# Kernel tuning notes

Hardware: AMD Instinct MI355X
Metric: run time of the kernel (lower is better)

## Reference

```python
import jax, jax.numpy as jnp
import numpy as np

EMBED_DIM = 1024
NUM_HEADS = 16
HEAD_DIM = EMBED_DIM // NUM_HEADS
BATCH = 2
SEQ = 2048


def setup_inputs() -> dict:
    key = jax.random.key(0)
    ks = jax.random.split(key, 10)
    s = 1.0 / np.sqrt(EMBED_DIM)
    inp = {
        "query": jax.random.normal(ks[0], (BATCH, SEQ, EMBED_DIM), jnp.float32),
        # Linear weights stored as [in, out] (y = x @ W + b)
        "wq": jax.random.normal(ks[1], (EMBED_DIM, EMBED_DIM), jnp.float32) * s,
        "bq": jnp.zeros((EMBED_DIM,), jnp.float32),
        "wk": jax.random.normal(ks[2], (EMBED_DIM, EMBED_DIM), jnp.float32) * s,
        "bk": jnp.zeros((EMBED_DIM,), jnp.float32),
        "wv": jax.random.normal(ks[3], (EMBED_DIM, EMBED_DIM), jnp.float32) * s,
        "bv": jnp.zeros((EMBED_DIM,), jnp.float32),
        "wo": jax.random.normal(ks[4], (EMBED_DIM, EMBED_DIM), jnp.float32) * s,
        "bo": jnp.zeros((EMBED_DIM,), jnp.float32),
        "temperature": jnp.float32(HEAD_DIM),  # learnable temperature, init = head_dim
    }
    return inp


def reference(query, wq, bq, wk, bk, wv, bv, wo, bo, temperature):
    B, S, E = query.shape
    # self-attention: key = value = query
    Q = (query @ wq + bq).reshape(B, S, NUM_HEADS, HEAD_DIM).transpose(0, 2, 1, 3)
    K = (query @ wk + bk).reshape(B, S, NUM_HEADS, HEAD_DIM).transpose(0, 2, 1, 3)
    V = (query @ wv + bv).reshape(B, S, NUM_HEADS, HEAD_DIM).transpose(0, 2, 1, 3)
    # squared Euclidean distances: ||q||^2 + ||k||^2 - 2<q,k>
    q_sq = jnp.sum(Q * Q, axis=-1, keepdims=True)          # (B,H,Sq,1)
    k_sq = jnp.sum(K * K, axis=-1, keepdims=True)          # (B,H,Sk,1)
    qk = jnp.einsum("bhqd,bhkd->bhqk", Q, K)
    d_sq = jnp.maximum(q_sq + jnp.swapaxes(k_sq, -2, -1) - 2.0 * qk, 0.0)
    attn = jax.nn.softmax(-d_sq / temperature, axis=-1)    # (B,H,Sq,Sk)
    out = jnp.einsum("bhqk,bhkd->bhqd", attn, V)
    out = out.transpose(0, 2, 1, 3).reshape(B, S, E)
    return out @ wo + bo
```

## Files before the change

kernel.cpp:

```cpp
#include <hip/hip_runtime.h>
#include <stdint.h>
#include <stddef.h>


#define LOG2E 1.44269504088896f

typedef __attribute__((ext_vector_type(8))) short bf16x8;
typedef __attribute__((ext_vector_type(4))) short bf16x4;
typedef __attribute__((ext_vector_type(4))) float f32x4;
typedef __attribute__((ext_vector_type(4))) unsigned short u16x4;

__device__ __forceinline__ unsigned short f2b(float f) {
  union { float f; unsigned int u; } x; x.f = f;
  unsigned int u = x.u;
  u += 0x7fffu + ((u >> 16) & 1u);
  return (unsigned short)(u >> 16);
}
__device__ __forceinline__ float b2f(unsigned short s) {
  union { unsigned int u; float f; } x; x.u = ((unsigned int)s) << 16;
  return x.f;
}
__device__ __forceinline__ unsigned int fbits(float f) {
  union { float f; unsigned int u; } x; x.f = f; return x.u;
}

#define GLD_LDS(g, l) __builtin_amdgcn_global_load_lds( \
    (const __attribute__((address_space(1))) void*)(g), \
    (__attribute__((address_space(3))) void*)(l), 16, 0, 0)

__global__ void prep_kernel(const float* __restrict__ X,
                            const float* __restrict__ wq, const float* __restrict__ wk,
                            const float* __restrict__ wv, const float* __restrict__ wo,
                            unsigned short* __restrict__ Xb,
                            unsigned short* __restrict__ WTqkv, unsigned short* __restrict__ WTo) {
  int z = blockIdx.z;
  if (z == 4) {
    size_t base = ((size_t)(blockIdx.y * 16 + blockIdx.x)) * 16384;
    #pragma unroll
    for (int j = 0; j < 16; ++j) {
      size_t i = base + (size_t)(j * 256 + threadIdx.x) * 4;
      f32x4 v = *(const f32x4*)&X[i];
      u16x4 o;
      #pragma unroll
      for (int k = 0; k < 4; ++k) o[k] = f2b(v[k]);
      *(u16x4*)&Xb[i] = o;
    }
    return;
  }
  __shared__ float tile[64][65];
  const float* src = (z == 0) ? wq : (z == 1) ? wk : (z == 2) ? wv : wo;
  unsigned short* dst = (z < 3) ? (WTqkv + (size_t)z * 1024 * 1024) : WTo;
  int k0 = blockIdx.y * 64, n0 = blockIdx.x * 64;
  int rr = threadIdx.x >> 6, cc = threadIdx.x & 63;
  #pragma unroll
  for (int p = 0; p < 16; ++p) {
    int row = p * 4 + rr;
    tile[row][cc] = src[(size_t)(k0 + row) * 1024 + n0 + cc];
  }
  __syncthreads();
  #pragma unroll
  for (int p = 0; p < 16; ++p) {
    int row = p * 4 + rr;
    dst[(size_t)(n0 + row) * 1024 + k0 + cc] = f2b(tile[cc][row]);
  }
}

__global__ __launch_bounds__(256, 3) void gemm_qkv_kernel(
    const unsigned short* __restrict__ X, const unsigned short* __restrict__ WT,
    const float* __restrict__ bq, const float* __restrict__ bk, const float* __restrict__ bv,
    unsigned short* __restrict__ Qb, unsigned short* __restrict__ Kb,
    unsigned short* __restrict__ VTo, float* __restrict__ qs2, float* __restrict__ ks2) {
  __shared__ unsigned short As[2 * 128 * 32];
  __shared__ unsigned short Bs[2 * 128 * 32];
  const int t = threadIdx.x, w = t >> 6, lane = t & 63;
  const int r = lane & 15, q4 = lane >> 4;
  const int m0 = blockIdx.y * 128, n0 = blockIdx.x * 128;
  const int wr = (w >> 1) * 64, wc = (w & 1) * 64;
  const unsigned short* Xg = X + (size_t)m0 * 1024;
  const unsigned short* Wg = WT + (size_t)n0 * 1024;
  f32x4 acc[4][4] = {};
  for (int k0 = 0; k0 < 1024; k0 += 64) {
    #pragma unroll
    for (int g = 0; g < 4; ++g) {
      int slot = g * 256 + t;
      int kh = slot >> 9, row = (slot >> 2) & 127, ko = (slot & 3) * 8;
      GLD_LDS(Xg + (size_t)row * 1024 + k0 + kh * 32 + ko, &As[(g * 256 + w * 64) * 8]);
      GLD_LDS(Wg + (size_t)row * 1024 + k0 + kh * 32 + ko, &Bs[(g * 256 + w * 64) * 8]);
    }
    __syncthreads();
    #pragma unroll
    for (int kh = 0; kh < 2; ++kh) {
      bf16x8 af[4], bfr[4];
      #pragma unroll
      for (int mf = 0; mf < 4; ++mf)
        af[mf] = *(const bf16x8*)&As[kh * 4096 + (wr + mf * 16 + r) * 32 + q4 * 8];
      #pragma unroll
      for (int nf = 0; nf < 4; ++nf)
        bfr[nf] = *(const bf16x8*)&Bs[kh * 4096 + (wc + nf * 16 + r) * 32 + q4 * 8];
      #pragma unroll
      for (int mf = 0; mf < 4; ++mf)
        #pragma unroll
        for (int nf = 0; nf < 4; ++nf)
          acc[mf][nf] = __builtin_amdgcn_mfma_f32_16x16x32_bf16(af[mf], bfr[nf], acc[mf][nf], 0, 0, 0);
    }
    __syncthreads();
  }
  const int nblk = n0 >> 10;
  if (nblk < 2) {
    const float* bias = (nblk == 0) ? bq : bk;
    unsigned short* OutB = (nblk == 0) ? Qb : Kb;
    float* S2 = (nblk == 0) ? qs2 : ks2;
    const int nc0 = n0 & 1023;
    float s2a[4][4] = {};
    #pragma unroll
    for (int nf = 0; nf < 4; ++nf) {
      int n = nc0 + wc + nf * 16 + r;
      float bb = bias[n];
      #pragma unroll
      for (int mf = 0; mf < 4; ++mf) {
        int m = m0 + wr + mf * 16 + q4 * 4;
        f32x4 v = acc[mf][nf];
        #pragma unroll
        for (int i = 0; i < 4; ++i) {
          unsigned short os = f2b(v[i] + bb);
          OutB[(size_t)(m + i) * 1024 + n] = os;
          float xb = b2f(os);
          s2a[mf][i] += xb * xb;
        }
      }
    }
    #pragma unroll
    for (int mf = 0; mf < 4; ++mf)
      #pragma unroll
      for (int i = 0; i < 4; ++i) {
        float v = s2a[mf][i];
        v += __shfl_xor(v, 1, 64);
        v += __shfl_xor(v, 2, 64);
        v += __shfl_xor(v, 4, 64);
        v += __shfl_xor(v, 8, 64);
        s2a[mf][i] = v;
      }
    if (r == 0) {
      int hh = (nc0 + wc) >> 6;
      #pragma unroll
      for (int mf = 0; mf < 4; ++mf) {
        int m = m0 + wr + mf * 16 + q4 * 4;
        int bb2 = m >> 11, ss = m & 2047;
        #pragma unroll
        for (int i = 0; i < 4; ++i)
          S2[(size_t)(bb2 * 16 + hh) * 2048 + ss + i] = s2a[mf][i];
      }
    }
  } else {
    const int c0 = n0 - 2048;
    #pragma unroll
    for (int nf = 0; nf < 4; ++nf) {
      int c = c0 + wc + nf * 16 + r;
      float bb = bv[c];
      int h = c >> 6, d = c & 63;
      #pragma unroll
      for (int mf = 0; mf < 4; ++mf) {
        int m = m0 + wr + mf * 16 + q4 * 4;
        int b = m >> 11, s = m & 2047;
        f32x4 v = acc[mf][nf];
        u16x4 pk;
        #pragma unroll
        for (int i = 0; i < 4; ++i) pk[i] = f2b(v[i] + bb);
        *(u16x4*)&VTo[((size_t)((b * 16 + h) * 64 + d)) * 2048 + s] = pk;
      }
    }
  }
}

__global__ __launch_bounds__(256, 2) void flash_kernel(
    const unsigned short* __restrict__ Qb, const unsigned short* __restrict__ Kb,
    const unsigned short* __restrict__ VT, const float* __restrict__ qs2,
    const float* __restrict__ ks2, const float* __restrict__ temp,
    unsigned short* __restrict__ AO) {
  __shared__ unsigned short Ks[2][64 * 64];
  __shared__ unsigned short Vs[2][64 * 64];
  const int t = threadIdx.x, w = t >> 6, lane = t & 63;
  const int r = lane & 15, q4 = lane >> 4;
  const int bh = blockIdx.y, b = bh >> 4, h = bh & 15;
  const int q0 = blockIdx.x * 128;
  const float scale = LOG2E / temp[0];
  const float cc = 2.0f * scale;

  bf16x8 qf[2][2];
  #pragma unroll
  for (int mf = 0; mf < 2; ++mf) {
    int sq = q0 + w * 32 + mf * 16 + r;
    const unsigned short* qp = Qb + (size_t)(b * 2048 + sq) * 1024 + h * 64;
    #pragma unroll
    for (int ks = 0; ks < 2; ++ks) qf[mf][ks] = *(const bf16x8*)(qp + ks * 32 + q4 * 8);
  }
  float qs_s[2];
  #pragma unroll
  for (int mf = 0; mf < 2; ++mf)
    qs_s[mf] = scale * qs2[bh * 2048 + q0 + w * 32 + mf * 16 + r];

  f32x4 accO[2][4] = {};
  f32x4 lsum[2] = {};
  bf16x8 ones;
  #pragma unroll
  for (int j = 0; j < 8; ++j) ones[j] = (short)0x3F80;

  const unsigned short* Kg = Kb + ((size_t)b * 2048) * 1024 + h * 64;
  const unsigned short* Vg = VT + ((size_t)bh * 64) * 2048;
  const float* kqb = ks2 + bh * 2048;

  #pragma unroll
  for (int g = 0; g < 2; ++g) {
    int slot = g * 256 + t;
    int khalf = slot >> 8, key = (slot >> 2) & 63, ko = (slot & 3) * 8;
    GLD_LDS(Kg + (size_t)key * 1024 + khalf * 32 + ko, &Ks[0][slot * 8]);
    int dd = slot >> 3, gg = (slot & 7) ^ (dd & 7);
    GLD_LDS(Vg + (size_t)dd * 2048 + gg * 8, &Vs[0][slot * 8]);
  }
  f32x4 kq[4];
  #pragma unroll
  for (int kfm = 0; kfm < 4; ++kfm) {
    f32x4 raw = *(const f32x4*)&kqb[kfm * 16 + q4 * 4];
    #pragma unroll
    for (int i = 0; i < 4; ++i) kq[kfm][i] = scale * raw[i];
  }

  #pragma unroll 2
  for (int c = 0; c < 32; ++c) {
    const int buf = c & 1;
    __syncthreads();
    f32x4 kqn[4];
    if (c < 31) {
      #pragma unroll
      for (int g = 0; g < 2; ++g) {
        int slot = g * 256 + t;
        int khalf = slot >> 8, key = (slot >> 2) & 63, ko = (slot & 3) * 8;
        GLD_LDS(Kg + (size_t)((c + 1) * 64 + key) * 1024 + khalf * 32 + ko,
                &Ks[buf ^ 1][slot * 8]);
        int dd = slot >> 3, gg = (slot & 7) ^ (dd & 7);
        GLD_LDS(Vg + (size_t)dd * 2048 + (c + 1) * 64 + gg * 8,
                &Vs[buf ^ 1][slot * 8]);
      }
      #pragma unroll
      for (int kfm = 0; kfm < 4; ++kfm) {
        f32x4 raw = *(const f32x4*)&kqb[(c + 1) * 64 + kfm * 16 + q4 * 4];
        #pragma unroll
        for (int i = 0; i < 4; ++i) kqn[kfm][i] = scale * raw[i];
      }
    }

    f32x4 accST[4][2] = {};
    #pragma unroll
    for (int ks = 0; ks < 2; ++ks) {
      #pragma unroll
      for (int kfm = 0; kfm < 4; ++kfm) {
        bf16x8 ka = *(const bf16x8*)&Ks[buf][(ks * 64 + kfm * 16 + r) * 32 + q4 * 8];
        accST[kfm][0] = __builtin_amdgcn_mfma_f32_16x16x32_bf16(ka, qf[0][ks], accST[kfm][0], 0, 0, 0);
        accST[kfm][1] = __builtin_amdgcn_mfma_f32_16x16x32_bf16(ka, qf[1][ks], accST[kfm][1], 0, 0, 0);
      }
    }

    bf16x8 pf[2][2];
    #pragma unroll
    for (int cb = 0; cb < 2; ++cb) {
      #pragma unroll
      for (int mf = 0; mf < 2; ++mf) {
        unsigned int dw[4];
        #pragma unroll
        for (int half = 0; half < 2; ++half) {
          int kfm = cb * 2 + half;
          float pp[4];
          #pragma unroll
          for (int i = 0; i < 4; ++i) {
            float u = __builtin_fmaf(cc, accST[kfm][mf][i], -(kq[kfm][i] + qs_s[mf]));
            pp[i] = __builtin_amdgcn_exp2f(fminf(u, 0.f));
          }
          dw[half * 2 + 0] = (fbits(pp[0]) >> 16) | (fbits(pp[1]) & 0xFFFF0000u);
          dw[half * 2 + 1] = (fbits(pp[2]) >> 16) | (fbits(pp[3]) & 0xFFFF0000u);
        }
        union { unsigned int d[4]; bf16x8 v; } cv;
        cv.d[0] = dw[0]; cv.d[1] = dw[1]; cv.d[2] = dw[2]; cv.d[3] = dw[3];
        pf[cb][mf] = cv.v;
      }
    }

    #pragma unroll
    for (int cb = 0; cb < 2; ++cb) {
      #pragma unroll
      for (int mf = 0; mf < 2; ++mf)
        lsum[mf] = __builtin_amdgcn_mfma_f32_16x16x32_bf16(pf[cb][mf], ones, lsum[mf], 0, 0, 0);
      #pragma unroll
      for (int df = 0; df < 4; ++df) {
        int dloc = df * 16 + r;
        int e0 = (cb * 4 + (q4 >> 1)) ^ (r & 7);
        int e1 = (cb * 4 + 2 + (q4 >> 1)) ^ (r & 7);
        bf16x4 v0 = *(const bf16x4*)&Vs[buf][dloc * 64 + e0 * 8 + (q4 & 1) * 4];
        bf16x4 v1 = *(const bf16x4*)&Vs[buf][dloc * 64 + e1 * 8 + (q4 & 1) * 4];
        bf16x8 vb = __builtin_shufflevector(v0, v1, 0, 1, 2, 3, 4, 5, 6, 7);
        #pragma unroll
        for (int mf = 0; mf < 2; ++mf)
          accO[mf][df] = __builtin_amdgcn_mfma_f32_16x16x32_bf16(pf[cb][mf], vb, accO[mf][df], 0, 0, 0);
      }
    }
    if (c < 31) {
      #pragma unroll
      for (int kfm = 0; kfm < 4; ++kfm) kq[kfm] = kqn[kfm];
    }
  }
  #pragma unroll
  for (int mf = 0; mf < 2; ++mf) {
    float inv[4];
    #pragma unroll
    for (int i = 0; i < 4; ++i) inv[i] = 1.0f / lsum[mf][i];
    #pragma unroll
    for (int df = 0; df < 4; ++df) {
      int d = df * 16 + r;
      #pragma unroll
      for (int i = 0; i < 4; ++i) {
        int sq = q0 + w * 32 + mf * 16 + q4 * 4 + i;
        AO[(size_t)(b * 2048 + sq) * 1024 + h * 64 + d] = f2b(accO[mf][df][i] * inv[i]);
      }
    }
  }
}

__global__ __launch_bounds__(256, 2) void gemm_out_kernel(
    const unsigned short* __restrict__ A, const unsigned short* __restrict__ WT,
    const float* __restrict__ bo, float* __restrict__ Out) {
  __shared__ unsigned short As[2 * 128 * 32];
  __shared__ unsigned short Bs[2 * 64 * 32];
  const int t = threadIdx.x, w = t >> 6, lane = t & 63;
  const int r = lane & 15, q4 = lane >> 4;
  const int m0 = blockIdx.y * 128, n0 = blockIdx.x * 64;
  const int wr = (w >> 1) * 64, wc = (w & 1) * 32;
  const unsigned short* Ag = A + (size_t)m0 * 1024;
  const unsigned short* Wg = WT + (size_t)n0 * 1024;
  f32x4 acc[4][2] = {};
  for (int k0 = 0; k0 < 1024; k0 += 64) {
    #pragma unroll
    for (int g = 0; g < 4; ++g) {
      int slot = g * 256 + t;
      int kh = slot >> 9, row = (slot >> 2) & 127, ko = (slot & 3) * 8;
      GLD_LDS(Ag + (size_t)row * 1024 + k0 + kh * 32 + ko, &As[(g * 256 + w * 64) * 8]);
    }
    #pragma unroll
    for (int g = 0; g < 2; ++g) {
      int slot = g * 256 + t;
      int kh = slot >> 8, row = (slot >> 2) & 63, ko = (slot & 3) * 8;
      GLD_LDS(Wg + (size_t)row * 1024 + k0 + kh * 32 + ko, &Bs[(g * 256 + w * 64) * 8]);
    }
    __syncthreads();
    #pragma unroll
    for (int kh = 0; kh < 2; ++kh) {
      bf16x8 af[4], bfr[2];
      #pragma unroll
      for (int mf = 0; mf < 4; ++mf)
        af[mf] = *(const bf16x8*)&As[kh * 4096 + (wr + mf * 16 + r) * 32 + q4 * 8];
      #pragma unroll
      for (int nf = 0; nf < 2; ++nf)
        bfr[nf] = *(const bf16x8*)&Bs[kh * 2048 + (wc + nf * 16 + r) * 32 + q4 * 8];
      #pragma unroll
      for (int mf = 0; mf < 4; ++mf)
        #pragma unroll
        for (int nf = 0; nf < 2; ++nf)
          acc[mf][nf] = __builtin_amdgcn_mfma_f32_16x16x32_bf16(af[mf], bfr[nf], acc[mf][nf], 0, 0, 0);
    }
    __syncthreads();
  }
  #pragma unroll
  for (int nf = 0; nf < 2; ++nf) {
    int n = n0 + wc + nf * 16 + r;
    float bb = bo[n];
    #pragma unroll
    for (int mf = 0; mf < 4; ++mf) {
      int m = m0 + wr + mf * 16 + q4 * 4;
      f32x4 v = acc[mf][nf];
      #pragma unroll
      for (int i = 0; i < 4; ++i)
        Out[(size_t)(m + i) * 1024 + n] = v[i] + bb;
    }
  }
}

extern "C" void kernel_launch(void* const* d_in, const int* in_sizes, int n_in,
                              void* d_out, int out_size, void* d_ws, size_t ws_size,
                              hipStream_t stream) {
  const float* X    = (const float*)d_in[0];
  const float* wq   = (const float*)d_in[1];
  const float* bq   = (const float*)d_in[2];
  const float* wk   = (const float*)d_in[3];
  const float* bk   = (const float*)d_in[4];
  const float* wv   = (const float*)d_in[5];
  const float* bv   = (const float*)d_in[6];
  const float* wo   = (const float*)d_in[7];
  const float* bo   = (const float*)d_in[8];
  const float* temp = (const float*)d_in[9];
  float* Out = (float*)d_out;

  char* ws = (char*)d_ws;
  unsigned short* Xb    = (unsigned short*)ws; ws += (size_t)4096 * 1024 * 2;
  unsigned short* WTqkv = (unsigned short*)ws; ws += (size_t)3072 * 1024 * 2;
  unsigned short* WTo   = (unsigned short*)ws; ws += (size_t)1024 * 1024 * 2;
  unsigned short* Qb    = (unsigned short*)ws; ws += (size_t)4096 * 1024 * 2;
  unsigned short* Kb    = (unsigned short*)ws; ws += (size_t)4096 * 1024 * 2;
  unsigned short* VT    = (unsigned short*)ws; ws += (size_t)4096 * 1024 * 2;
  unsigned short* AO    = (unsigned short*)ws; ws += (size_t)4096 * 1024 * 2;
  float* qs2 = (float*)ws; ws += (size_t)65536 * 4;
  float* ks2 = (float*)ws; ws += (size_t)65536 * 4;

  prep_kernel<<<dim3(16, 16, 5), 256, 0, stream>>>(X, wq, wk, wv, wo, Xb, WTqkv, WTo);
  gemm_qkv_kernel<<<dim3(24, 32), 256, 0, stream>>>(Xb, WTqkv, bq, bk, bv, Qb, Kb, VT, qs2, ks2);
  flash_kernel<<<dim3(16, 32), 256, 0, stream>>>(Qb, Kb, VT, qs2, ks2, temp, AO);
  gemm_out_kernel<<<dim3(16, 32), 256, 0, stream>>>(AO, WTo, bo, Out);
}
```

Baseline: 208.5 us.

## Permute V layout via LDS staging for single 16-byte V loads in flash

The V epilogue of the QKV GEMM now stages its tile in shared memory with a permuted key order. It then writes each V^T row with coalesced 8-byte stores instead of scattered strided ones. Because of that permutation, the flash kernel can fetch each V fragment with one 16-byte LDS read instead of two 8-byte reads plus a shuffle. The softmax scale is folded into the q/k squared-norm outputs of the GEMM, which removes per-tile multiplies in flash, and AO now reuses the Xb buffer. The risk is that the key permutation in the stored V must match exactly the P fragment ordering used in the PV MFMA.

Measured after the change: 203.2 us. 2.5% less time.

```diff
diff --git a/kernel.cpp b/kernel.cpp
--- a/kernel.cpp
+++ b/kernel.cpp
@@ -6,9 +6,9 @@
 #define LOG2E 1.44269504088896f
 
 typedef __attribute__((ext_vector_type(8))) short bf16x8;
-typedef __attribute__((ext_vector_type(4))) short bf16x4;
 typedef __attribute__((ext_vector_type(4))) float f32x4;
 typedef __attribute__((ext_vector_type(4))) unsigned short u16x4;
+typedef __attribute__((ext_vector_type(8))) unsigned short u16x8;
 
 __device__ __forceinline__ unsigned short f2b(float f) {
   union { float f; unsigned int u; } x; x.f = f;
@@ -68,10 +68,12 @@
 __global__ __launch_bounds__(256, 3) void gemm_qkv_kernel(
     const unsigned short* __restrict__ X, const unsigned short* __restrict__ WT,
     const float* __restrict__ bq, const float* __restrict__ bk, const float* __restrict__ bv,
+    const float* __restrict__ temp,
     unsigned short* __restrict__ Qb, unsigned short* __restrict__ Kb,
     unsigned short* __restrict__ VTo, float* __restrict__ qs2, float* __restrict__ ks2) {
-  __shared__ unsigned short As[2 * 128 * 32];
-  __shared__ unsigned short Bs[2 * 128 * 32];
+  __shared__ __align__(16) unsigned short smem[16896];
+  unsigned short* As = smem;
+  unsigned short* Bs = smem + 8192;
   const int t = threadIdx.x, w = t >> 6, lane = t & 63;
   const int r = lane & 15, q4 = lane >> 4;
   const int m0 = blockIdx.y * 128, n0 = blockIdx.x * 128;
@@ -110,6 +112,7 @@
     const float* bias = (nblk == 0) ? bq : bk;
     unsigned short* OutB = (nblk == 0) ? Qb : Kb;
     float* S2 = (nblk == 0) ? qs2 : ks2;
+    const float sc = LOG2E / temp[0];
     const int nc0 = n0 & 1023;
     float s2a[4][4] = {};
     #pragma unroll
@@ -138,7 +141,7 @@
         v += __shfl_xor(v, 2, 64);
         v += __shfl_xor(v, 4, 64);
         v += __shfl_xor(v, 8, 64);
-        s2a[mf][i] = v;
+        s2a[mf][i] = v * sc;
       }
     if (r == 0) {
       int hh = (nc0 + wc) >> 6;
@@ -152,23 +155,37 @@
       }
     }
   } else {
+    unsigned short* Vt = smem;
     const int c0 = n0 - 2048;
+    const int head = w & 1;
     #pragma unroll
     for (int nf = 0; nf < 4; ++nf) {
       int c = c0 + wc + nf * 16 + r;
       float bb = bv[c];
-      int h = c >> 6, d = c & 63;
+      int d = c & 63;
       #pragma unroll
       for (int mf = 0; mf < 4; ++mf) {
-        int m = m0 + wr + mf * 16 + q4 * 4;
-        int b = m >> 11, s = m & 2047;
+        int mloc = wr + mf * 16 + q4 * 4;
+        int G = mloc >> 6;
+        int k6 = mloc & 63;
+        int pos = (k6 >> 5) * 32 + ((k6 & 15) >> 2) * 8 + ((k6 >> 4) & 1) * 4;
         f32x4 v = acc[mf][nf];
         u16x4 pk;
         #pragma unroll
         for (int i = 0; i < 4; ++i) pk[i] = f2b(v[i] + bb);
-        *(u16x4*)&VTo[((size_t)((b * 16 + h) * 64 + d)) * 2048 + s] = pk;
-      }
-    }
+        *(u16x4*)&Vt[(head * 64 + d) * 132 + G * 64 + pos] = pk;
+      }
+    }
+    __syncthreads();
+    int row = t >> 1, ch = t & 1;
+    int hd = row >> 6, dd = row & 63;
+    int hglob = (c0 >> 6) + hd;
+    int bb2 = m0 >> 11, s0 = m0 & 2047;
+    unsigned short* dst = &VTo[((size_t)((bb2 * 16 + hglob) * 64 + dd)) * 2048 + s0 + ch * 64];
+    const unsigned short* srcL = &Vt[(hd * 64 + dd) * 132 + ch * 64];
+    #pragma unroll
+    for (int k2 = 0; k2 < 16; ++k2)
+      *(u16x4*)&dst[k2 * 4] = *(const u16x4*)&srcL[k2 * 4];
   }
 }
 
@@ -177,14 +194,13 @@
     const unsigned short* __restrict__ VT, const float* __restrict__ qs2,
     const float* __restrict__ ks2, const float* __restrict__ temp,
     unsigned short* __restrict__ AO) {
-  __shared__ unsigned short Ks[2][64 * 64];
-  __shared__ unsigned short Vs[2][64 * 64];
+  __shared__ __align__(16) unsigned short Ks[2][64 * 64];
+  __shared__ __align__(16) unsigned short Vs[2][64 * 64];
   const int t = threadIdx.x, w = t >> 6, lane = t & 63;
   const int r = lane & 15, q4 = lane >> 4;
   const int bh = blockIdx.y, b = bh >> 4, h = bh & 15;
   const int q0 = blockIdx.x * 128;
-  const float scale = LOG2E / temp[0];
-  const float cc = 2.0f * scale;
+  const float cc = 2.0f * LOG2E / temp[0];
 
   bf16x8 qf[2][2];
   #pragma unroll
@@ -197,7 +213,7 @@
   float qs_s[2];
   #pragma unroll
   for (int mf = 0; mf < 2; ++mf)
-    qs_s[mf] = scale * qs2[bh * 2048 + q0 + w * 32 + mf * 16 + r];
+    qs_s[mf] = qs2[bh * 2048 + q0 + w * 32 + mf * 16 + r];
 
   f32x4 accO[2][4] = {};
   f32x4 lsum[2] = {};
@@ -214,16 +230,13 @@
     int slot = g * 256 + t;
     int khalf = slot >> 8, key = (slot >> 2) & 63, ko = (slot & 3) * 8;
     GLD_LDS(Kg + (size_t)key * 1024 + khalf * 32 + ko, &Ks[0][slot * 8]);
-    int dd = slot >> 3, gg = (slot & 7) ^ (dd & 7);
-    GLD_LDS(Vg + (size_t)dd * 2048 + gg * 8, &Vs[0][slot * 8]);
+    int dd = slot >> 3, pb = (slot & 7) ^ (dd & 7);
+    GLD_LDS(Vg + (size_t)dd * 2048 + pb * 8, &Vs[0][slot * 8]);
   }
   f32x4 kq[4];
   #pragma unroll
-  for (int kfm = 0; kfm < 4; ++kfm) {
-    f32x4 raw = *(const f32x4*)&kqb[kfm * 16 + q4 * 4];
-    #pragma unroll
-    for (int i = 0; i < 4; ++i) kq[kfm][i] = scale * raw[i];
-  }
+  for (int kfm = 0; kfm < 4; ++kfm)
+    kq[kfm] = *(const f32x4*)&kqb[kfm * 16 + q4 * 4];
 
   #pragma unroll 2
   for (int c = 0; c < 32; ++c) {
@@ -237,16 +250,13 @@
         int khalf = slot >> 8, key = (slot >> 2) & 63, ko = (slot & 3) * 8;
         GLD_LDS(Kg + (size_t)((c + 1) * 64 + key) * 1024 + khalf * 32 + ko,
                 &Ks[buf ^ 1][slot * 8]);
-        int dd = slot >> 3, gg = (slot & 7) ^ (dd & 7);
-        GLD_LDS(Vg + (size_t)dd * 2048 + (c + 1) * 64 + gg * 8,
+        int dd = slot >> 3, pb = (slot & 7) ^ (dd & 7);
+        GLD_LDS(Vg + (size_t)dd * 2048 + (c + 1) * 64 + pb * 8,
                 &Vs[buf ^ 1][slot * 8]);
       }
       #pragma unroll
-      for (int kfm = 0; kfm < 4; ++kfm) {
-        f32x4 raw = *(const f32x4*)&kqb[(c + 1) * 64 + kfm * 16 + q4 * 4];
-        #pragma unroll
-        for (int i = 0; i < 4; ++i) kqn[kfm][i] = scale * raw[i];
-      }
+      for (int kfm = 0; kfm < 4; ++kfm)
+        kqn[kfm] = *(const f32x4*)&kqb[(c + 1) * 64 + kfm * 16 + q4 * 4];
     }
 
     f32x4 accST[4][2] = {};
@@ -292,11 +302,8 @@
       #pragma unroll
       for (int df = 0; df < 4; ++df) {
         int dloc = df * 16 + r;
-        int e0 = (cb * 4 + (q4 >> 1)) ^ (r & 7);
-        int e1 = (cb * 4 + 2 + (q4 >> 1)) ^ (r & 7);
-        bf16x4 v0 = *(const bf16x4*)&Vs[buf][dloc * 64 + e0 * 8 + (q4 & 1) * 4];
-        bf16x4 v1 = *(const bf16x4*)&Vs[buf][dloc * 64 + e1 * 8 + (q4 & 1) * 4];
-        bf16x8 vb = __builtin_shufflevector(v0, v1, 0, 1, 2, 3, 4, 5, 6, 7);
+        int un = dloc * 8 + ((cb * 4 + q4) ^ (dloc & 7));
+        bf16x8 vb = *(const bf16x8*)&Vs[buf][un * 8];
         #pragma unroll
         for (int mf = 0; mf < 2; ++mf)
           accO[mf][df] = __builtin_amdgcn_mfma_f32_16x16x32_bf16(pf[cb][mf], vb, accO[mf][df], 0, 0, 0);
@@ -327,8 +334,8 @@
 __global__ __launch_bounds__(256, 2) void gemm_out_kernel(
     const unsigned short* __restrict__ A, const unsigned short* __restrict__ WT,
     const float* __restrict__ bo, float* __restrict__ Out) {
-  __shared__ unsigned short As[2 * 128 * 32];
-  __shared__ unsigned short Bs[2 * 64 * 32];
+  __shared__ __align__(16) unsigned short As[2 * 128 * 32];
+  __shared__ __align__(16) unsigned short Bs[2 * 64 * 32];
   const int t = threadIdx.x, w = t >> 6, lane = t & 63;
   const int r = lane & 15, q4 = lane >> 4;
   const int m0 = blockIdx.y * 128, n0 = blockIdx.x * 64;
@@ -404,12 +411,12 @@
   unsigned short* Qb    = (unsigned short*)ws; ws += (size_t)4096 * 1024 * 2;
   unsigned short* Kb    = (unsigned short*)ws; ws += (size_t)4096 * 1024 * 2;
   unsigned short* VT    = (unsigned short*)ws; ws += (size_t)4096 * 1024 * 2;
-  unsigned short* AO    = (unsigned short*)ws; ws += (size_t)4096 * 1024 * 2;
   float* qs2 = (float*)ws; ws += (size_t)65536 * 4;
   float* ks2 = (float*)ws; ws += (size_t)65536 * 4;
+  unsigned short* AO = Xb;
 
   prep_kernel<<<dim3(16, 16, 5), 256, 0, stream>>>(X, wq, wk, wv, wo, Xb, WTqkv, WTo);
-  gemm_qkv_kernel<<<dim3(24, 32), 256, 0, stream>>>(Xb, WTqkv, bq, bk, bv, Qb, Kb, VT, qs2, ks2);
+  gemm_qkv_kernel<<<dim3(24, 32), 256, 0, stream>>>(Xb, WTqkv, bq, bk, bv, temp, Qb, Kb, VT, qs2, ks2);
   flash_kernel<<<dim3(16, 32), 256, 0, stream>>>(Qb, Kb, VT, qs2, ks2, temp, AO);
   gemm_out_kernel<<<dim3(16, 32), 256, 0, stream>>>(AO, WTo, bo, Out);
 }
```
